# Performance work log

Measured on AMD Instinct MI355X. Metric: run time of the kernel, lower is better.

The kernel has to match this reference:

```python
import jax, jax.numpy as jnp
import numpy as np

SCALE = 1.0
STEPS = 5
ALIGN_CORNERS = True
SHAPE = (2, 3, 128, 128, 128)  # N, C(=3 vector comps), D, H, W


def _identity_grid(spatial, align_corners):
    # spatial = (D, H, W); returns [D, H, W, 3] with coords ordered (x, y, z) in [-1, 1],
    # matching torch.nn.functional.grid_sample's grid convention.
    axes = []
    for s in spatial:
        if align_corners:
            axes.append(jnp.linspace(-1.0, 1.0, s, dtype=jnp.float32))
        else:
            axes.append(((2.0 * jnp.arange(s, dtype=jnp.float32) + 1.0) / s) - 1.0)
    zz, yy, xx = jnp.meshgrid(axes[0], axes[1], axes[2], indexing="ij")  # each [D,H,W]
    return jnp.stack([xx, yy, zz], axis=-1)


def _grid_sample_3d(u, grid, align_corners):
    # u: [N, D, H, W, C] channels-last values; grid: [N, D, H, W, 3] (x, y, z) in [-1, 1].
    # Trilinear interpolation with border padding (deepali expv default: PaddingMode.BORDER).
    N, D, H, W, C = u.shape

    def unnorm(g, size):
        if align_corners:
            return (g + 1.0) * 0.5 * (size - 1)
        return ((g + 1.0) * size - 1.0) * 0.5

    x = jnp.clip(unnorm(grid[..., 0], W), 0.0, W - 1)
    y = jnp.clip(unnorm(grid[..., 1], H), 0.0, H - 1)
    z = jnp.clip(unnorm(grid[..., 2], D), 0.0, D - 1)

    x0f, y0f, z0f = jnp.floor(x), jnp.floor(y), jnp.floor(z)
    wx = (x - x0f)[..., None]  # [N,D,H,W,1]
    wy = (y - y0f)[..., None]
    wz = (z - z0f)[..., None]

    x0 = x0f.astype(jnp.int32); x1 = jnp.minimum(x0 + 1, W - 1)
    y0 = y0f.astype(jnp.int32); y1 = jnp.minimum(y0 + 1, H - 1)
    z0 = z0f.astype(jnp.int32); z1 = jnp.minimum(z0 + 1, D - 1)

    b = jnp.arange(N)[:, None, None, None]  # broadcast batch index [N,1,1,1]

    def gather(zi, yi, xi):
        return u[b, zi, yi, xi]  # [N,D,H,W,C]

    # interpolate along x, then y, then z
    c00 = gather(z0, y0, x0) * (1 - wx) + gather(z0, y0, x1) * wx
    c01 = gather(z0, y1, x0) * (1 - wx) + gather(z0, y1, x1) * wx
    c10 = gather(z1, y0, x0) * (1 - wx) + gather(z1, y0, x1) * wx
    c11 = gather(z1, y1, x0) * (1 - wx) + gather(z1, y1, x1) * wx
    c0 = c00 * (1 - wy) + c01 * wy
    c1 = c10 * (1 - wy) + c11 * wy
    return c0 * (1 - wz) + c1 * wz


def setup_inputs() -> dict:
    key = jax.random.key(0)
    # velocity field: small displacements in normalized cube coordinates
    x = jax.random.normal(key, SHAPE, dtype=jnp.float32) * 0.1
    return {"x": x}


def reference(x) -> jnp.ndarray:
    # expv: scaling-and-squaring exponentiation of velocity field x -> displacement field.
    # u <- scale * x / 2^steps; repeat steps times: u <- u + u o u  (self-composition via warp)
    scale = SCALE / (2 ** STEPS)
    u = jnp.moveaxis(x, 1, -1) * scale  # [N, D, H, W, 3], channels (x, y, z)
    grid0 = _identity_grid(x.shape[2:], ALIGN_CORNERS)  # [D, H, W, 3]
    for _ in range(STEPS):
        u = u + _grid_sample_3d(u, grid0[None] + u, ALIGN_CORNERS)
    return jnp.moveaxis(u, -1, 1)  # back to [N, 3, D, H, W]
```

## Files before the change

### kernel.cpp

```cpp
#include <hip/hip_runtime.h>


namespace {
constexpr int kD = 128, kH = 128, kW = 128, kN = 2, kC = 3;
constexpr int kPlane = kD * kH * kW;
constexpr int kVol   = kC * kPlane;
constexpr int kTotalVox   = kN * kPlane;
constexpr int kTotalElems = kN * kVol;
constexpr size_t kBatchBytes = (size_t)kPlane * 6;
constexpr float kScale0 = 1.0f / 32.0f;
}

typedef float f32x2 __attribute__((ext_vector_type(2)));
typedef unsigned int u32;
typedef u32 u32x3 __attribute__((ext_vector_type(3), aligned(4)));
typedef u32 u32x4a4 __attribute__((ext_vector_type(4), aligned(4)));

static __device__ __forceinline__ float h2f(u32 bits) {
    _Float16 v;
    unsigned short s = (unsigned short)bits;
    __builtin_memcpy(&v, &s, 2);
    return (float)v;
}
static __device__ __forceinline__ u32 f2h2(float a, float b) {
    _Float16 ha = (_Float16)a, hb = (_Float16)b;
    unsigned short sa, sb;
    __builtin_memcpy(&sa, &ha, 2);
    __builtin_memcpy(&sb, &hb, 2);
    return (u32)sa | ((u32)sb << 16);
}

static __device__ __forceinline__ int slab_rr(int* n_out, bool rev) {
    int b    = blockIdx.x;
    int xcd  = b & 7;
    int seq  = b >> 3;
    if (rev) seq = 1023 - seq;
    int slab = xcd | ((seq >> 9) << 3);
    *n_out   = slab >> 3;
    int dblk = slab & 7;
    int vo   = ((seq & 511) << 9) | (threadIdx.x << 1);
    return (dblk << 18) | vo;
}

__global__ __launch_bounds__(256) void transcode_kernel(const float* __restrict__ x,
                                                        void* __restrict__ aos) {
    int n;
    int rr = slab_rr(&n, false);
    const float* __restrict__ ub = x + (size_t)n * kVol;
    f32x2 bx = *(const f32x2*)(ub + rr);
    f32x2 by = *(const f32x2*)(ub + kPlane + rr);
    f32x2 bz = *(const f32x2*)(ub + 2 * kPlane + rr);
    bx *= kScale0; by *= kScale0; bz *= kScale0;
    u32x3 s;
    s.x = f2h2(bx.x, by.x);
    s.y = f2h2(bz.x, bz.y);
    s.z = f2h2(bx.y, by.y);
    char* ob = (char*)aos + (size_t)n * kBatchBytes;
    *(u32x3*)(ob + (size_t)(rr >> 1) * 12) = s;
}

template <int MODE, bool REV>
__global__ __launch_bounds__(256) void step_p6h(const void* __restrict__ uin,
                                                void* __restrict__ uout) {
    int n;
    int rr = slab_rr(&n, REV);
    int w = rr & 127;
    int h = (rr >> 7) & 127;
    int d = rr >> 14;

    const char* __restrict__ ubase = (const char*)uin + (size_t)n * kBatchBytes;

    u32x3 bq = *(const u32x3*)(ubase + (size_t)(rr >> 1) * 12);
    float vx[2], vy[2], vz[2];
    vx[0] = h2f(bq.x & 0xffffu); vy[0] = h2f(bq.x >> 16); vz[0] = h2f(bq.y & 0xffffu);
    vx[1] = h2f(bq.z & 0xffffu); vy[1] = h2f(bq.z >> 16); vz[1] = h2f(bq.y >> 16);

    int   o[2];
    float wxa[2], wya[2], wza[2];
    #pragma unroll
    for (int j = 0; j < 2; ++j) {
        float px = fminf(fmaxf((float)(w + j) + vx[j] * 63.5f, 0.0f), 127.0f);
        float py = fminf(fmaxf((float)h       + vy[j] * 63.5f, 0.0f), 127.0f);
        float pz = fminf(fmaxf((float)d       + vz[j] * 63.5f, 0.0f), 127.0f);
        int x0 = min((int)floorf(px), 126);
        int y0 = min((int)floorf(py), 126);
        int z0 = min((int)floorf(pz), 126);
        wxa[j] = px - (float)x0;
        wya[j] = py - (float)y0;
        wza[j] = pz - (float)z0;
        o[j] = (z0 << 14) + (y0 << 7) + x0;
    }

    const int rowbyte[4] = {0, 768, 98304, 99072};
    float res[3][2];
    #pragma unroll
    for (int j = 0; j < 2; ++j) {
        float wx = wxa[j], wy = wya[j], wz = wza[j];
        float omx = 1.0f - wx, omy = 1.0f - wy, omz = 1.0f - wz;
        u32 pb = (u32)(o[j] & 1);
        size_t gb = (size_t)(o[j] >> 1) * 12 + (pb << 2);
        float cr[4][3];
        #pragma unroll
        for (int r = 0; r < 4; ++r) {
            u32x4a4 q = *(const u32x4a4*)(ubase + gb + rowbyte[r]);
            u32 xy0 = pb ? q.y : q.x;
            u32 z0b = pb ? (q.x >> 16) : (q.y & 0xffffu);
            u32 xy1 = q.z;
            u32 z1b = pb ? (q.w & 0xffffu) : (q.y >> 16);
            float ax = h2f(xy0 & 0xffffu), ay = h2f(xy0 >> 16), az = h2f(z0b);
            float bx = h2f(xy1 & 0xffffu), by = h2f(xy1 >> 16), bz = h2f(z1b);
            cr[r][0] = ax * omx + bx * wx;
            cr[r][1] = ay * omx + by * wx;
            cr[r][2] = az * omx + bz * wx;
        }
        #pragma unroll
        for (int c = 0; c < 3; ++c) {
            float c0 = cr[0][c] * omy + cr[1][c] * wy;
            float c1 = cr[2][c] * omy + cr[3][c] * wy;
            float base = (c == 0) ? vx[j] : (c == 1) ? vy[j] : vz[j];
            res[c][j] = base + (c0 * omz + c1 * wz);
        }
    }

    if constexpr (MODE == 2) {
        float* __restrict__ obp = (float*)uout + (size_t)n * kVol;
        *(f32x2*)(obp + rr)              = f32x2{res[0][0], res[0][1]};
        *(f32x2*)(obp + kPlane + rr)     = f32x2{res[1][0], res[1][1]};
        *(f32x2*)(obp + 2 * kPlane + rr) = f32x2{res[2][0], res[2][1]};
    } else {
        u32x3 s;
        s.x = f2h2(res[0][0], res[1][0]);
        s.y = f2h2(res[2][0], res[2][1]);
        s.z = f2h2(res[0][1], res[1][1]);
        char* ob = (char*)uout + (size_t)n * kBatchBytes;
        *(u32x3*)(ob + (size_t)(rr >> 1) * 12) = s;
    }
}

template <bool SCALED>
__global__ __launch_bounds__(256) void step_kernel(const float* __restrict__ u,
                                                   float* __restrict__ out) {
    int b    = blockIdx.x;
    int xcd  = b & 7;
    int seq  = b >> 3;
    int slab = xcd | ((seq >> 9) << 3);
    int n    = slab >> 3;
    int dblk = slab & 7;
    int vo   = ((seq & 511) << 9) | (threadIdx.x << 1);
    int rr   = (dblk << 18) | vo;

    int w = rr & 127;
    int h = (rr >> 7) & 127;
    int d = rr >> 14;

    const float* __restrict__ ub = u + (size_t)n * kVol;

    f32x2 bx = *(const f32x2*)(ub + rr);
    f32x2 by = *(const f32x2*)(ub + kPlane + rr);
    f32x2 bz = *(const f32x2*)(ub + 2 * kPlane + rr);
    if (SCALED) { bx *= kScale0; by *= kScale0; bz *= kScale0; }

    int   o[2];
    float wxa[2], wya[2], wza[2];
    #pragma unroll
    for (int j = 0; j < 2; ++j) {
        float vx = (j == 0) ? bx.x : bx.y;
        float vy = (j == 0) ? by.x : by.y;
        float vz = (j == 0) ? bz.x : bz.y;
        float px = fminf(fmaxf((float)(w + j) + vx * 63.5f, 0.0f), 127.0f);
        float py = fminf(fmaxf((float)h       + vy * 63.5f, 0.0f), 127.0f);
        float pz = fminf(fmaxf((float)d       + vz * 63.5f, 0.0f), 127.0f);
        int x0 = min((int)floorf(px), 126);
        int y0 = min((int)floorf(py), 126);
        int z0 = min((int)floorf(pz), 126);
        wxa[j] = px - (float)x0;
        wya[j] = py - (float)y0;
        wza[j] = pz - (float)z0;
        o[j] = (z0 << 14) + (y0 << 7) + x0;
    }

    const int rowoff[4] = {0, 128, 16384, 16512};
    float res[3][2];
    #pragma unroll
    for (int j = 0; j < 2; ++j) {
        float wx = wxa[j], wy = wya[j], wz = wza[j];
        float omx = 1.0f - wx, omy = 1.0f - wy, omz = 1.0f - wz;
        #pragma unroll
        for (int c = 0; c < 3; ++c) {
            const float* __restrict__ up = ub + c * kPlane;
            f32x2 v00 = *(const f32x2*)(up + o[j] + rowoff[0]);
            f32x2 v01 = *(const f32x2*)(up + o[j] + rowoff[1]);
            f32x2 v10 = *(const f32x2*)(up + o[j] + rowoff[2]);
            f32x2 v11 = *(const f32x2*)(up + o[j] + rowoff[3]);
            if (SCALED) { v00 *= kScale0; v01 *= kScale0; v10 *= kScale0; v11 *= kScale0; }
            float c00 = v00.x * omx + v00.y * wx;
            float c01 = v01.x * omx + v01.y * wx;
            float c10 = v10.x * omx + v10.y * wx;
            float c11 = v11.x * omx + v11.y * wx;
            float c0 = c00 * omy + c01 * wy;
            float c1 = c10 * omy + c11 * wy;
            float s  = c0 * omz + c1 * wz;
            float base = (c == 0) ? ((j == 0) ? bx.x : bx.y)
                       : (c == 1) ? ((j == 0) ? by.x : by.y)
                                  : ((j == 0) ? bz.x : bz.y);
            res[c][j] = base + s;
        }
    }

    float* __restrict__ ob = out + (size_t)n * kVol;
    *(f32x2*)(ob + rr)              = f32x2{res[0][0], res[0][1]};
    *(f32x2*)(ob + kPlane + rr)     = f32x2{res[1][0], res[1][1]};
    *(f32x2*)(ob + 2 * kPlane + rr) = f32x2{res[2][0], res[2][1]};
}

extern "C" void kernel_launch(void* const* d_in, const int* in_sizes, int n_in,
                              void* d_out, int out_size, void* d_ws, size_t ws_size,
                              hipStream_t stream) {
    const float* x = (const float*)d_in[0];
    float* out = (float*)d_out;

    const int grd = kTotalVox / (256 * 2);
    const size_t need_p6 = (size_t)2 * kN * kBatchBytes + 4096;

    if (ws_size >= need_p6) {
        char* A = (char*)d_ws;
        char* B = A + (size_t)kN * kBatchBytes;
        transcode_kernel<<<grd, 256, 0, stream>>>(x, A);
        step_p6h<1, true ><<<grd, 256, 0, stream>>>(A, B);
        step_p6h<1, false><<<grd, 256, 0, stream>>>(B, A);
        step_p6h<1, true ><<<grd, 256, 0, stream>>>(A, B);
        step_p6h<1, false><<<grd, 256, 0, stream>>>(B, A);
        step_p6h<2, true ><<<grd, 256, 0, stream>>>(A, out);
    } else {
        float* ws = (float*)d_ws;
        step_kernel<true ><<<grd, 256, 0, stream>>>(x,   out);
        step_kernel<false><<<grd, 256, 0, stream>>>(out, ws);
        step_kernel<false><<<grd, 256, 0, stream>>>(ws,  out);
        step_kernel<false><<<grd, 256, 0, stream>>>(out, ws);
        step_kernel<false><<<grd, 256, 0, stream>>>(ws,  out);
    }
}
```

Before: 206.0 us.

## Use 3D-tiled 1024-thread blocks and nontemporal I/O for the fp16 AoS step path

Voxel-to-thread mapping changes from flat 512-voxel rows to 1024-thread blocks covering a 128(w)x4(h)x4(d) brick, so the gathers in each block hit a more compact 3D neighbourhood and get better cache reuse. Launch size goes to 1024 threads and the grid shrinks to match. The fp32 input load in transcode and the final fp32 output store now use nontemporal hints so streamed data does not pollute the cache. The larger blocks can lower occupancy or scheduling flexibility, and the fallback path keeps 256-thread launches.

```diff
diff --git a/kernel.cpp b/kernel.cpp
--- a/kernel.cpp
+++ b/kernel.cpp
@@ -34,22 +34,29 @@
     int b    = blockIdx.x;
     int xcd  = b & 7;
     int seq  = b >> 3;
-    if (rev) seq = 1023 - seq;
-    int slab = xcd | ((seq >> 9) << 3);
+    if (rev) seq = 255 - seq;
+    int slab = xcd | (((seq >> 7) & 1) << 3);
     *n_out   = slab >> 3;
     int dblk = slab & 7;
-    int vo   = ((seq & 511) << 9) | (threadIdx.x << 1);
-    return (dblk << 18) | vo;
-}
-
-__global__ __launch_bounds__(256) void transcode_kernel(const float* __restrict__ x,
-                                                        void* __restrict__ aos) {
+    int s7   = seq & 127;
+    int ht   = s7 & 31;
+    int dt   = (s7 >> 5) & 3;
+    int wl   = threadIdx.x & 63;
+    int hh   = (threadIdx.x >> 6) & 3;
+    int dd   = (threadIdx.x >> 8) & 3;
+    int d    = (dblk << 4) | (dt << 2) | dd;
+    int h    = (ht << 2) | hh;
+    return (d << 14) | (h << 7) | (wl << 1);
+}
+
+__global__ __launch_bounds__(1024) void transcode_kernel(const float* __restrict__ x,
+                                                         void* __restrict__ aos) {
     int n;
     int rr = slab_rr(&n, false);
     const float* __restrict__ ub = x + (size_t)n * kVol;
-    f32x2 bx = *(const f32x2*)(ub + rr);
-    f32x2 by = *(const f32x2*)(ub + kPlane + rr);
-    f32x2 bz = *(const f32x2*)(ub + 2 * kPlane + rr);
+    f32x2 bx = __builtin_nontemporal_load((const f32x2*)(ub + rr));
+    f32x2 by = __builtin_nontemporal_load((const f32x2*)(ub + kPlane + rr));
+    f32x2 bz = __builtin_nontemporal_load((const f32x2*)(ub + 2 * kPlane + rr));
     bx *= kScale0; by *= kScale0; bz *= kScale0;
     u32x3 s;
     s.x = f2h2(bx.x, by.x);
@@ -60,8 +67,8 @@
 }
 
 template <int MODE, bool REV>
-__global__ __launch_bounds__(256) void step_p6h(const void* __restrict__ uin,
-                                                void* __restrict__ uout) {
+__global__ __launch_bounds__(1024) void step_p6h(const void* __restrict__ uin,
+                                                 void* __restrict__ uout) {
     int n;
     int rr = slab_rr(&n, REV);
     int w = rr & 127;
@@ -124,9 +131,9 @@
 
     if constexpr (MODE == 2) {
         float* __restrict__ obp = (float*)uout + (size_t)n * kVol;
-        *(f32x2*)(obp + rr)              = f32x2{res[0][0], res[0][1]};
-        *(f32x2*)(obp + kPlane + rr)     = f32x2{res[1][0], res[1][1]};
-        *(f32x2*)(obp + 2 * kPlane + rr) = f32x2{res[2][0], res[2][1]};
+        __builtin_nontemporal_store(f32x2{res[0][0], res[0][1]}, (f32x2*)(obp + rr));
+        __builtin_nontemporal_store(f32x2{res[1][0], res[1][1]}, (f32x2*)(obp + kPlane + rr));
+        __builtin_nontemporal_store(f32x2{res[2][0], res[2][1]}, (f32x2*)(obp + 2 * kPlane + rr));
     } else {
         u32x3 s;
         s.x = f2h2(res[0][0], res[1][0]);
@@ -219,24 +226,25 @@
     const float* x = (const float*)d_in[0];
     float* out = (float*)d_out;
 
-    const int grd = kTotalVox / (256 * 2);
+    const int grd = kTotalVox / (1024 * 2);
     const size_t need_p6 = (size_t)2 * kN * kBatchBytes + 4096;
 
     if (ws_size >= need_p6) {
         char* A = (char*)d_ws;
         char* B = A + (size_t)kN * kBatchBytes;
-        transcode_kernel<<<grd, 256, 0, stream>>>(x, A);
-        step_p6h<1, true ><<<grd, 256, 0, stream>>>(A, B);
-        step_p6h<1, false><<<grd, 256, 0, stream>>>(B, A);
-        step_p6h<1, true ><<<grd, 256, 0, stream>>>(A, B);
-        step_p6h<1, false><<<grd, 256, 0, stream>>>(B, A);
-        step_p6h<2, true ><<<grd, 256, 0, stream>>>(A, out);
+        transcode_kernel<<<grd, 1024, 0, stream>>>(x, A);
+        step_p6h<1, true ><<<grd, 1024, 0, stream>>>(A, B);
+        step_p6h<1, false><<<grd, 1024, 0, stream>>>(B, A);
+        step_p6h<1, true ><<<grd, 1024, 0, stream>>>(A, B);
+        step_p6h<1, false><<<grd, 1024, 0, stream>>>(B, A);
+        step_p6h<2, true ><<<grd, 1024, 0, stream>>>(A, out);
     } else {
         float* ws = (float*)d_ws;
-        step_kernel<true ><<<grd, 256, 0, stream>>>(x,   out);
-        step_kernel<false><<<grd, 256, 0, stream>>>(out, ws);
-        step_kernel<false><<<grd, 256, 0, stream>>>(ws,  out);
-        step_kernel<false><<<grd, 256, 0, stream>>>(out, ws);
-        step_kernel<false><<<grd, 256, 0, stream>>>(ws,  out);
-    }
-}
+        const int g256 = kTotalVox / (256 * 2);
+        step_kernel<true ><<<g256, 256, 0, stream>>>(x,   out);
+        step_kernel<false><<<g256, 256, 0, stream>>>(out, ws);
+        step_kernel<false><<<g256, 256, 0, stream>>>(ws,  out);
+        step_kernel<false><<<g256, 256, 0, stream>>>(out, ws);
+        step_kernel<false><<<g256, 256, 0, stream>>>(ws,  out);
+    }
+}
```

New measurement: 202.5 us, median of 2. No clear change (-1.7%).
